# Optimization experiments

Hardware: AMD Instinct MI355X
Metric: run time of the kernel (lower is better)

## Reference

```python
import jax, jax.numpy as jnp
import numpy as np

H = 8
DK = 64          # d_model // h
D_MODEL = 512
DIM_G = 64       # trignometric geometry embedding dim
WAVE_LEN = 1000.0


def box_relational_embedding(boxes):
    # boxes: [B, N, 4] = (x_min, y_min, x_max, y_max)
    x_min, y_min, x_max, y_max = [boxes[..., i:i + 1] for i in range(4)]  # each [B,N,1]
    cx = (x_min + x_max) * 0.5
    cy = (y_min + y_max) * 0.5
    w = (x_max - x_min) + 1.0
    h = (y_max - y_min) + 1.0

    def rel(c, s):
        # log(clamp(|c_i - c_j| / s_i, 1e-3)) -> [B,N,N]
        return jnp.log(jnp.clip(jnp.abs((c - jnp.swapaxes(c, -2, -1)) / s), 1e-3, None))

    delta_x = rel(cx, w)
    delta_y = rel(cy, h)
    delta_w = jnp.log(w / jnp.swapaxes(w, -2, -1))
    delta_h = jnp.log(h / jnp.swapaxes(h, -2, -1))
    pos = jnp.stack([delta_x, delta_y, delta_w, delta_h], axis=-1)  # [B,N,N,4]

    n_freq = DIM_G // 8  # 8 frequencies per geometric feature
    feat_range = jnp.arange(n_freq, dtype=pos.dtype)
    dim_mat = 1.0 / (WAVE_LEN ** (feat_range / n_freq))            # [n_freq]
    mul = (100.0 * pos)[..., None] * dim_mat                        # [B,N,N,4,n_freq]
    B, N = pos.shape[0], pos.shape[1]
    mul = mul.reshape(B, N, N, 4 * n_freq)                          # [B,N,N,32]
    return jnp.concatenate([jnp.sin(mul), jnp.cos(mul)], axis=-1)   # [B,N,N,64]


def setup_inputs() -> dict:
    key = jax.random.key(0)
    ks = jax.random.split(key, 14)
    B, N = 4, 512
    s = 0.02
    return {
        "input_query": jax.random.normal(ks[0], (B, N, D_MODEL), jnp.float32),
        "input_key":   jax.random.normal(ks[1], (B, N, D_MODEL), jnp.float32),
        "input_value": jax.random.normal(ks[2], (B, N, D_MODEL), jnp.float32),
        "input_box":   jax.random.uniform(ks[3], (B, N, 4), jnp.float32),
        "Wq": jax.random.normal(ks[4], (D_MODEL, D_MODEL), jnp.float32) * s,
        "bq": jax.random.normal(ks[5], (D_MODEL,), jnp.float32) * s,
        "Wk": jax.random.normal(ks[6], (D_MODEL, D_MODEL), jnp.float32) * s,
        "bk": jax.random.normal(ks[7], (D_MODEL,), jnp.float32) * s,
        "Wv": jax.random.normal(ks[8], (D_MODEL, D_MODEL), jnp.float32) * s,
        "bv": jax.random.normal(ks[9], (D_MODEL,), jnp.float32) * s,
        "Wo": jax.random.normal(ks[10], (D_MODEL, D_MODEL), jnp.float32) * s,
        "bo": jax.random.normal(ks[11], (D_MODEL,), jnp.float32) * s,
        "WG": jax.random.normal(ks[12], (H, DIM_G), jnp.float32) * s,
        "bG": jax.random.normal(ks[13], (H,), jnp.float32) * s,
    }


def reference(input_query, input_key, input_value, input_box,
              Wq, bq, Wk, bk, Wv, bv, Wo, bo, WG, bG):
    B, N, _ = input_query.shape

    # geometry log-bias per head: relu(Linear_h(emb)) -> [B,H,N,N]
    emb = box_relational_embedding(input_box)                        # [B,N,N,64]
    wg = jax.nn.relu(jnp.einsum('bmng,hg->bhmn', emb, WG)
                     + bG[None, :, None, None])

    def proj(x, W, b):
        # torch Linear: x @ W^T + b, then split heads -> [B,H,N,DK]
        y = x @ W.T + b
        return y.reshape(B, N, H, DK).transpose(0, 2, 1, 3)

    q = proj(input_query, Wq, bq)
    k = proj(input_key, Wk, bk)
    v = proj(input_value, Wv, bv)

    scale = 1.0 / jnp.sqrt(jnp.asarray(DK, q.dtype))
    scores = jnp.einsum('bhqd,bhkd->bhqk', q, k) * scale             # [B,H,N,N]
    logits = jnp.log(jnp.clip(wg, 1e-6, None)) + scores
    attn = jax.nn.softmax(logits, axis=-1)                           # dropout is identity in eval
    out = jnp.einsum('bhqk,bhkd->bhqd', attn, v)
    out = out.transpose(0, 2, 1, 3).reshape(B, N, H * DK)
    return out @ Wo.T + bo
```

## Files before the change

kernel.cpp:

```cpp
#include <hip/hip_runtime.h>
#include <hip/hip_bf16.h>
#include <cstdint>

typedef unsigned short u16;
typedef unsigned int u32;
typedef __attribute__((ext_vector_type(8))) short short8;
typedef __attribute__((ext_vector_type(4))) float f32x4;
typedef __attribute__((ext_vector_type(4))) unsigned int u32x4;
typedef __attribute__((ext_vector_type(4))) unsigned short u16x4;

#define REV 15.91549431f

__device__ __forceinline__ u16 f2b(float x) { return __builtin_bit_cast(u16, (__bf16)x); }
__device__ __forceinline__ u16 f2h(float x) { return __builtin_bit_cast(u16, (_Float16)x); }
__device__ __forceinline__ float c_dim_f(int f) {
    const float c[8] = {1.0f, 0.42169650f, 0.17782794f, 0.074989421f,
                        0.031622777f, 0.013335214f, 0.0056234132f, 0.0023713737f};
    return c[f];
}
__device__ __forceinline__ void gload_lds16(const void* g, void* l) {
    __builtin_amdgcn_global_load_lds((const __attribute__((address_space(1))) u32*)g,
                                     (__attribute__((address_space(3))) u32*)l, 16, 0, 0);
}

__global__ __launch_bounds__(256) void prep_k(const float* __restrict__ s0,
                                              const float* __restrict__ s1,
                                              const float* __restrict__ s2,
                                              const float* __restrict__ s3,
                                              const float* __restrict__ s4,
                                              const float* __restrict__ s5,
                                              const float* __restrict__ s6,
                                              const float* __restrict__ box,
                                              const float* __restrict__ WG,
                                              const float* __restrict__ bG,
                                              u16* __restrict__ dstX,
                                              u16* __restrict__ dstW,
                                              u16* __restrict__ outW) {
    __shared__ char embs[256 * 128];
    const int z = blockIdx.z;
    const int t = threadIdx.x;

    if (z < 7) {
        const float* s;
        u16* dst;
        if (z < 3) {
            s = (z == 0) ? s0 : (z == 1) ? s1 : s2;
            dst = dstX + (size_t)z * 1048576;
        } else {
            if (blockIdx.x >= 256) return;
            s = (z == 3) ? s3 : (z == 4) ? s4 : (z == 5) ? s5 : s6;
            dst = dstW + (size_t)(z - 3) * 262144;
        }
        int i = (blockIdx.x * 256 + t) * 4;
        float4 v = *(const float4*)&s[i];
        u16x4 o = { f2b(v.x), f2b(v.y), f2b(v.z), f2b(v.w) };
        *(u16x4*)&dst[i] = o;
        return;
    }

    if (blockIdx.x >= 256) return;
    const int wave = t >> 6, lane = t & 63;
    const int b = z - 7;
    const int ipair = blockIdx.x;
    const int swz = (t & 7) << 4;

    float cxi[2], cyi[2], wdi[2], hgi[2], lwi[2], lhi[2];
#pragma unroll
    for (int iu = 0; iu < 2; iu++) {
        int ii = (ipair << 1) + iu;
        float4 bi = *(const float4*)&box[(size_t)(((b << 9) + ii) << 2)];
        cxi[iu] = (bi.x + bi.z) * 0.5f; cyi[iu] = (bi.y + bi.w) * 0.5f;
        wdi[iu] = bi.z - bi.x + 1.0f;   hgi[iu] = bi.w - bi.y + 1.0f;
        lwi[iu] = __logf(wdi[iu]);      lhi[iu] = __logf(hgi[iu]);
    }

    const int hh = lane & 15;
    const int ko = (lane >> 4) << 3;
    short8 bf0 = {0,0,0,0,0,0,0,0}, bf1 = {0,0,0,0,0,0,0,0};
    float bGh = 0.0f;
    if (hh < 8) {
        const float* wrow = WG + hh * 64;
#pragma unroll
        for (int e = 0; e < 8; e++) {
            bf0[e] = (short)f2b(wrow[ko + e]);
            bf1[e] = (short)f2b(wrow[32 + ko + e]);
        }
        bGh = bG[hh];
    }

    for (int jt = 0; jt < 2; jt++) {
        const int j = (jt << 8) + t;
        float4 bj = *(const float4*)&box[(size_t)(((b << 9) + j) << 2)];
        float cxj = (bj.x + bj.z) * 0.5f, cyj = (bj.y + bj.w) * 0.5f;
        float wdj = bj.z - bj.x + 1.0f,   hgj = bj.w - bj.y + 1.0f;
        float lwj = __logf(wdj), lhj = __logf(hgj);

#pragma unroll
        for (int iu = 0; iu < 2; iu++) {
            const int ii = (ipair << 1) + iu;
            float pos[4];
            pos[0] = __logf(fmaxf(fabsf((cxi[iu] - cxj) / wdi[iu]), 1e-3f));
            pos[1] = __logf(fmaxf(fabsf((cyi[iu] - cyj) / hgi[iu]), 1e-3f));
            pos[2] = lwi[iu] - lwj;
            pos[3] = lhi[iu] - lhj;

#pragma unroll
            for (int p = 0; p < 4; p++) {
                float rev = pos[p] * REV;
                u32x4 sp, cp;
#pragma unroll
                for (int f = 0; f < 4; f++) {
                    float a0 = rev * c_dim_f(2 * f), a1 = rev * c_dim_f(2 * f + 1);
                    sp[f] = (u32)f2b(__builtin_amdgcn_sinf(a0)) | ((u32)f2b(__builtin_amdgcn_sinf(a1)) << 16);
                    cp[f] = (u32)f2b(__builtin_amdgcn_cosf(a0)) | ((u32)f2b(__builtin_amdgcn_cosf(a1)) << 16);
                }
                *(u32x4*)(embs + (((t << 7) + (p << 4)) ^ swz)) = sp;
                *(u32x4*)(embs + (((t << 7) + 64 + (p << 4)) ^ swz)) = cp;
            }
            __syncthreads();

#pragma unroll
            for (int tt = 0; tt < 4; tt++) {
                int mt = (wave << 2) + tt;
                int row = (mt << 4) + hh;
                int rswz = (row & 7) << 4;
                short8 a0v = *(const short8*)(embs + (((row << 7) + (ko << 1)) ^ rswz));
                short8 a1v = *(const short8*)(embs + (((row << 7) + 64 + (ko << 1)) ^ rswz));
                f32x4 acc = {0.f, 0.f, 0.f, 0.f};
                acc = __builtin_amdgcn_mfma_f32_16x16x32_bf16(a0v, bf0, acc, 0, 0, 0);
                acc = __builtin_amdgcn_mfma_f32_16x16x32_bf16(a1v, bf1, acc, 0, 0, 0);
                if (hh < 8) {
                    int j0 = (jt << 8) + (mt << 4) + ((lane >> 4) << 2);
                    u16x4 ow;
#pragma unroll
                    for (int r = 0; r < 4; r++)
                        ow[r] = f2h(fmaxf(acc[r] + bGh, 1e-6f) * 1024.0f);
                    *(u16x4*)&outW[((size_t)((b << 3) + hh) << 18) + ((size_t)ii << 9) + j0] = ow;
                }
            }
            __syncthreads();
        }
    }
}

__global__ __launch_bounds__(256) void attn_k(const u16* __restrict__ Qb,
                                              const u16* __restrict__ Kb,
                                              const u16* __restrict__ VT,
                                              const u16* __restrict__ Wp,
                                              u16* __restrict__ ATT) {
    __shared__ u16 Pl[4][16 * 68];
    __shared__ float Mrg[3][64][25];
    const int t = threadIdx.x;
    const int wave = t >> 6, lane = t & 63;
    const int c = lane & 15, g = lane >> 4;
    const int bid = blockIdx.x;
    const int qb = bid & 31, bh = bid >> 5;
    const int b = bh >> 3, h = bh & 7;
    const int q0 = qb << 4;

    const u16* Qp = Qb + ((size_t)bh << 15);
    const u16* Kp = Kb + ((size_t)bh << 15);
    const u16* Vp = VT + ((size_t)bh << 15);
    const _Float16* Bp = (const _Float16*)Wp + ((size_t)bh << 18) + ((size_t)q0 << 9);

    short8 qf[2];
#pragma unroll
    for (int ks = 0; ks < 2; ks++)
        qf[ks] = *(const short8*)&Qp[(size_t)(q0 + c) * 64 + ks * 32 + g * 8];

    f32x4 o[4] = {};
    float m[4] = {-1e30f, -1e30f, -1e30f, -1e30f};
    float l[4] = {0.f, 0.f, 0.f, 0.f};

    for (int kt = 0; kt < 2; kt++) {
        const int k0 = ((wave << 1) + kt) << 6;
        short8 kf[4][2], vf[4][2];
#pragma unroll
        for (int jj = 0; jj < 4; jj++)
#pragma unroll
            for (int ks = 0; ks < 2; ks++) {
                kf[jj][ks] = *(const short8*)&Kp[(size_t)(k0 + jj * 16 + c) * 64 + ks * 32 + g * 8];
                vf[jj][ks] = *(const short8*)&Vp[(size_t)(jj * 16 + c) * 512 + k0 + ks * 32 + g * 8];
            }
        float wgt[4][4];
#pragma unroll
        for (int jj = 0; jj < 4; jj++)
#pragma unroll
            for (int r = 0; r < 4; r++)
                wgt[jj][r] = (float)Bp[(size_t)(g * 4 + r) * 512 + k0 + jj * 16 + c];

        f32x4 sa[4] = {};
        __builtin_amdgcn_s_setprio(1);
#pragma unroll
        for (int jj = 0; jj < 4; jj++)
#pragma unroll
            for (int ks = 0; ks < 2; ks++)
                sa[jj] = __builtin_amdgcn_mfma_f32_16x16x32_bf16(qf[ks], kf[jj][ks], sa[jj], 0, 0, 0);
        __builtin_amdgcn_s_setprio(0);

        float s[4][4];
#pragma unroll
        for (int r = 0; r < 4; r++) {
#pragma unroll
            for (int jj = 0; jj < 4; jj++)
                s[jj][r] = sa[jj][r] * 0.125f;
            float v = fmaxf(fmaxf(s[0][r], s[1][r]), fmaxf(s[2][r], s[3][r]));
#pragma unroll
            for (int off = 1; off < 16; off <<= 1)
                v = fmaxf(v, __shfl_xor(v, off));
            float mn = fmaxf(m[r], v);
            float alpha = __expf(m[r] - mn);
            m[r] = mn;
            float rs = 0.f;
#pragma unroll
            for (int jj = 0; jj < 4; jj++) {
                float p = wgt[jj][r] * __expf(s[jj][r] - mn);
                s[jj][r] = p;
                rs += p;
            }
#pragma unroll
            for (int off = 1; off < 16; off <<= 1)
                rs += __shfl_xor(rs, off);
            l[r] = l[r] * alpha + rs;
#pragma unroll
            for (int jjo = 0; jjo < 4; jjo++)
                o[jjo][r] *= alpha;
        }

#pragma unroll
        for (int jj = 0; jj < 4; jj++)
#pragma unroll
            for (int r = 0; r < 4; r++)
                Pl[wave][(g * 4 + r) * 68 + jj * 16 + c] = f2b(s[jj][r]);
        asm volatile("s_waitcnt lgkmcnt(0)" ::: "memory");
        __builtin_amdgcn_sched_barrier(0);

        short8 pa[2];
#pragma unroll
        for (int ks = 0; ks < 2; ks++)
            pa[ks] = *(const short8*)&Pl[wave][c * 68 + ks * 32 + g * 8];
        __builtin_amdgcn_s_setprio(1);
#pragma unroll
        for (int jjo = 0; jjo < 4; jjo++)
#pragma unroll
            for (int ks = 0; ks < 2; ks++)
                o[jjo] = __builtin_amdgcn_mfma_f32_16x16x32_bf16(pa[ks], vf[jjo][ks], o[jjo], 0, 0, 0);
        __builtin_amdgcn_s_setprio(0);
        __builtin_amdgcn_sched_barrier(0);
    }

    if (wave > 0) {
#pragma unroll
        for (int r = 0; r < 4; r++) {
            Mrg[wave - 1][lane][r] = m[r];
            Mrg[wave - 1][lane][4 + r] = l[r];
#pragma unroll
            for (int jjo = 0; jjo < 4; jjo++)
                Mrg[wave - 1][lane][8 + jjo * 4 + r] = o[jjo][r];
        }
    }
    __syncthreads();
    if (wave == 0) {
#pragma unroll
        for (int w = 0; w < 3; w++) {
#pragma unroll
            for (int r = 0; r < 4; r++) {
                float m1 = Mrg[w][lane][r];
                float l1 = Mrg[w][lane][4 + r];
                float mn = fmaxf(m[r], m1);
                float a0 = __expf(m[r] - mn), a1 = __expf(m1 - mn);
                m[r] = mn;
                l[r] = l[r] * a0 + l1 * a1;
#pragma unroll
                for (int jjo = 0; jjo < 4; jjo++)
                    o[jjo][r] = o[jjo][r] * a0 + Mrg[w][lane][8 + jjo * 4 + r] * a1;
            }
        }
#pragma unroll
        for (int r = 0; r < 4; r++) {
            float inv = 1.0f / l[r];
            int row = q0 + g * 4 + r;
#pragma unroll
            for (int jjo = 0; jjo < 4; jjo++)
                ATT[(size_t)(((b << 9) + row) << 9) + (h << 6) + jjo * 16 + c] = f2b(o[jjo][r] * inv);
        }
    }
}

__global__ __launch_bounds__(256) void proj_k(const u16* __restrict__ Xall,
                                              const u16* __restrict__ Wall,
                                              const float* __restrict__ bq,
                                              const float* __restrict__ bk,
                                              const float* __restrict__ bv,
                                              u16* __restrict__ Qb,
                                              u16* __restrict__ Kb,
                                              u16* __restrict__ VT) {
    __shared__ u16 As[2][64 * 32];
    __shared__ u16 Bs[2][64 * 32];

    const int t = threadIdx.x;
    const int wave = t >> 6, lane = t & 63;
    const int wr = wave >> 1, wc = wave & 1;
    const int m0 = blockIdx.y * 64, n0 = blockIdx.x * 64;
    const int z = blockIdx.z;

    const u16* A  = Xall + (size_t)z * 1048576;
    const u16* Bm = Wall + (size_t)z * 262144;
    const float* bias = (z == 0) ? bq : (z == 1) ? bk : bv;
    u16* out = (z == 0) ? Qb : (z == 1) ? Kb : VT;

    f32x4 acc[2][2] = {};
    const int srow = t >> 2;
    const int scol = (((t & 3) ^ ((t >> 3) & 3)) << 3);
    const int c = lane & 15, g = lane >> 4;
    const int gsw = (g ^ ((c >> 1) & 3)) << 3;

    const size_t arow = (size_t)(m0 + srow) * 512 + scol;
    const size_t brow = (size_t)(n0 + srow) * 512 + scol;

    gload_lds16(&A[arow], &As[0][t * 8]);
    gload_lds16(&Bm[brow], &Bs[0][t * 8]);

    int cur = 0;
    for (int k0 = 0; k0 < 512; k0 += 32, cur ^= 1) {
        if (k0 + 32 < 512) {
            gload_lds16(&A[arow + k0 + 32], &As[cur ^ 1][t * 8]);
            gload_lds16(&Bm[brow + k0 + 32], &Bs[cur ^ 1][t * 8]);
            asm volatile("s_waitcnt vmcnt(2)" ::: "memory");
        } else {
            asm volatile("s_waitcnt vmcnt(0)" ::: "memory");
        }
        __builtin_amdgcn_s_barrier();
        __builtin_amdgcn_sched_barrier(0);
        short8 af[2], bfr[2];
#pragma unroll
        for (int i = 0; i < 2; i++)
            af[i] = *(const short8*)&As[cur][(wr * 32 + i * 16 + c) * 32 + gsw];
#pragma unroll
        for (int jj = 0; jj < 2; jj++)
            bfr[jj] = *(const short8*)&Bs[cur][(wc * 32 + jj * 16 + c) * 32 + gsw];
#pragma unroll
        for (int i = 0; i < 2; i++)
#pragma unroll
            for (int jj = 0; jj < 2; jj++)
                acc[i][jj] = __builtin_amdgcn_mfma_f32_16x16x32_bf16(af[i], bfr[jj], acc[i][jj], 0, 0, 0);
        __builtin_amdgcn_sched_barrier(0);
        __builtin_amdgcn_s_barrier();
    }

#pragma unroll
    for (int i = 0; i < 2; i++)
#pragma unroll
        for (int jj = 0; jj < 2; jj++)
#pragma unroll
            for (int r = 0; r < 4; r++) {
                int row = m0 + wr * 32 + i * 16 + ((lane >> 4) << 2) + r;
                int col = n0 + wc * 32 + jj * 16 + (lane & 15);
                float v = acc[i][jj][r] + bias[col];
                int b = row >> 9, rr = row & 511, h = col >> 6, d = col & 63;
                if (z < 2)
                    out[(size_t)((((b << 3) + h) << 9) + rr) * 64 + d] = f2b(v);
                else
                    out[(size_t)((((b << 3) + h) << 6) + d) * 512 + rr] = f2b(v);
            }
}

__global__ __launch_bounds__(256) void outg_k(const u16* __restrict__ A,
                                              const u16* __restrict__ Bm,
                                              const float* __restrict__ bias,
                                              float* __restrict__ outF) {
    __shared__ u16 As[2][64 * 32];
    __shared__ u16 Bs[2][64 * 32];

    const int t = threadIdx.x;
    const int wave = t >> 6, lane = t & 63;
    const int wr = wave >> 1, wc = wave & 1;
    const int m0 = blockIdx.y * 64, n0 = blockIdx.x * 64;

    f32x4 acc[2][2] = {};
    const int srow = t >> 2;
    const int scol = (((t & 3) ^ ((t >> 3) & 3)) << 3);
    const int c = lane & 15, g = lane >> 4;
    const int gsw = (g ^ ((c >> 1) & 3)) << 3;

    const size_t arow = (size_t)(m0 + srow) * 512 + scol;
    const size_t brow = (size_t)(n0 + srow) * 512 + scol;

    gload_lds16(&A[arow], &As[0][t * 8]);
    gload_lds16(&Bm[brow], &Bs[0][t * 8]);

    int cur = 0;
    for (int k0 = 0; k0 < 512; k0 += 32, cur ^= 1) {
        if (k0 + 32 < 512) {
            gload_lds16(&A[arow + k0 + 32], &As[cur ^ 1][t * 8]);
            gload_lds16(&Bm[brow + k0 + 32], &Bs[cur ^ 1][t * 8]);
            asm volatile("s_waitcnt vmcnt(2)" ::: "memory");
        } else {
            asm volatile("s_waitcnt vmcnt(0)" ::: "memory");
        }
        __builtin_amdgcn_s_barrier();
        __builtin_amdgcn_sched_barrier(0);
        short8 af[2], bfr[2];
#pragma unroll
        for (int i = 0; i < 2; i++)
            af[i] = *(const short8*)&As[cur][(wr * 32 + i * 16 + c) * 32 + gsw];
#pragma unroll
        for (int jj = 0; jj < 2; jj++)
            bfr[jj] = *(const short8*)&Bs[cur][(wc * 32 + jj * 16 + c) * 32 + gsw];
#pragma unroll
        for (int i = 0; i < 2; i++)
#pragma unroll
            for (int jj = 0; jj < 2; jj++)
                acc[i][jj] = __builtin_amdgcn_mfma_f32_16x16x32_bf16(af[i], bfr[jj], acc[i][jj], 0, 0, 0);
        __builtin_amdgcn_sched_barrier(0);
        __builtin_amdgcn_s_barrier();
    }

#pragma unroll
    for (int i = 0; i < 2; i++)
#pragma unroll
        for (int jj = 0; jj < 2; jj++)
#pragma unroll
            for (int r = 0; r < 4; r++) {
                int row = m0 + wr * 32 + i * 16 + ((lane >> 4) << 2) + r;
                int col = n0 + wc * 32 + jj * 16 + (lane & 15);
                outF[((size_t)row << 9) + col] = acc[i][jj][r] + bias[col];
            }
}

extern "C" void kernel_launch(void* const* d_in, const int* in_sizes, int n_in,
                              void* d_out, int out_size, void* d_ws, size_t ws_size,
                              hipStream_t stream) {
    const float* inq = (const float*)d_in[0];
    const float* ink = (const float*)d_in[1];
    const float* inv = (const float*)d_in[2];
    const float* box = (const float*)d_in[3];
    const float* Wq  = (const float*)d_in[4];
    const float* bq  = (const float*)d_in[5];
    const float* Wk  = (const float*)d_in[6];
    const float* bk  = (const float*)d_in[7];
    const float* Wv  = (const float*)d_in[8];
    const float* bv  = (const float*)d_in[9];
    const float* Wo  = (const float*)d_in[10];
    const float* bo  = (const float*)d_in[11];
    const float* WG  = (const float*)d_in[12];
    const float* bG  = (const float*)d_in[13];

    u16* base = (u16*)d_ws;
    u16* Xall = base;
    u16* Wall = base + 3145728;
    u16* Qb   = base + 4194304;
    u16* Kb   = base + 5242880;
    u16* VT   = base + 6291456;
    u16* ATT  = base + 7340032;
    u16* Wp   = base + 8388608;

    prep_k<<<dim3(1024, 1, 11), 256, 0, stream>>>(inq, ink, inv, Wq, Wk, Wv, Wo,
                                                  box, WG, bG, Xall, Wall, Wp);

    proj_k<<<dim3(8, 32, 3), 256, 0, stream>>>(Xall, Wall, bq, bk, bv, Qb, Kb, VT);

    attn_k<<<dim3(1024), 256, 0, stream>>>(Qb, Kb, VT, Wp, ATT);

    outg_k<<<dim3(8, 32, 1), 256, 0, stream>>>(ATT, Wall + 786432, bo, (float*)d_out);
}
```

Before: 70.09 us.

## Use single-wave attention blocks that sweep all key tiles without cross-wave merge

The attention kernel now launches one 64-thread wave per query block instead of four waves splitting the key range. Each wave iterates over all eight key tiles with online softmax, which removes the LDS merge of partial max/sum/output and the block barrier. The cost is four times less parallelism per query block and a longer serial loop per wave, so fewer waves are in flight to hide memory latency.

Result: no change. 68.95 us (-1.6%).

```diff
diff --git a/kernel.cpp b/kernel.cpp
--- a/kernel.cpp
+++ b/kernel.cpp
@@ -143,15 +143,13 @@
     }
 }
 
-__global__ __launch_bounds__(256) void attn_k(const u16* __restrict__ Qb,
-                                              const u16* __restrict__ Kb,
-                                              const u16* __restrict__ VT,
-                                              const u16* __restrict__ Wp,
-                                              u16* __restrict__ ATT) {
-    __shared__ u16 Pl[4][16 * 68];
-    __shared__ float Mrg[3][64][25];
-    const int t = threadIdx.x;
-    const int wave = t >> 6, lane = t & 63;
+__global__ __launch_bounds__(64) void attn_k(const u16* __restrict__ Qb,
+                                             const u16* __restrict__ Kb,
+                                             const u16* __restrict__ VT,
+                                             const u16* __restrict__ Wp,
+                                             u16* __restrict__ ATT) {
+    __shared__ u16 Pl[16 * 68];
+    const int lane = threadIdx.x;
     const int c = lane & 15, g = lane >> 4;
     const int bid = blockIdx.x;
     const int qb = bid & 31, bh = bid >> 5;
@@ -172,8 +170,8 @@
     float m[4] = {-1e30f, -1e30f, -1e30f, -1e30f};
     float l[4] = {0.f, 0.f, 0.f, 0.f};
 
-    for (int kt = 0; kt < 2; kt++) {
-        const int k0 = ((wave << 1) + kt) << 6;
+    for (int kt = 0; kt < 8; kt++) {
+        const int k0 = kt << 6;
         short8 kf[4][2], vf[4][2];
 #pragma unroll
         for (int jj = 0; jj < 4; jj++)
@@ -231,14 +229,14 @@
         for (int jj = 0; jj < 4; jj++)
 #pragma unroll
             for (int r = 0; r < 4; r++)
-                Pl[wave][(g * 4 + r) * 68 + jj * 16 + c] = f2b(s[jj][r]);
+                Pl[(g * 4 + r) * 68 + jj * 16 + c] = f2b(s[jj][r]);
         asm volatile("s_waitcnt lgkmcnt(0)" ::: "memory");
         __builtin_amdgcn_sched_barrier(0);
 
         short8 pa[2];
 #pragma unroll
         for (int ks = 0; ks < 2; ks++)
-            pa[ks] = *(const short8*)&Pl[wave][c * 68 + ks * 32 + g * 8];
+            pa[ks] = *(const short8*)&Pl[c * 68 + ks * 32 + g * 8];
         __builtin_amdgcn_s_setprio(1);
 #pragma unroll
         for (int jjo = 0; jjo < 4; jjo++)
@@ -249,41 +247,13 @@
         __builtin_amdgcn_sched_barrier(0);
     }
 
-    if (wave > 0) {
-#pragma unroll
-        for (int r = 0; r < 4; r++) {
-            Mrg[wave - 1][lane][r] = m[r];
-            Mrg[wave - 1][lane][4 + r] = l[r];
-#pragma unroll
-            for (int jjo = 0; jjo < 4; jjo++)
-                Mrg[wave - 1][lane][8 + jjo * 4 + r] = o[jjo][r];
-        }
-    }
-    __syncthreads();
-    if (wave == 0) {
-#pragma unroll
-        for (int w = 0; w < 3; w++) {
-#pragma unroll
-            for (int r = 0; r < 4; r++) {
-                float m1 = Mrg[w][lane][r];
-                float l1 = Mrg[w][lane][4 + r];
-                float mn = fmaxf(m[r], m1);
-                float a0 = __expf(m[r] - mn), a1 = __expf(m1 - mn);
-                m[r] = mn;
-                l[r] = l[r] * a0 + l1 * a1;
-#pragma unroll
-                for (int jjo = 0; jjo < 4; jjo++)
-                    o[jjo][r] = o[jjo][r] * a0 + Mrg[w][lane][8 + jjo * 4 + r] * a1;
-            }
-        }
-#pragma unroll
-        for (int r = 0; r < 4; r++) {
-            float inv = 1.0f / l[r];
-            int row = q0 + g * 4 + r;
-#pragma unroll
-            for (int jjo = 0; jjo < 4; jjo++)
-                ATT[(size_t)(((b << 9) + row) << 9) + (h << 6) + jjo * 16 + c] = f2b(o[jjo][r] * inv);
-        }
+#pragma unroll
+    for (int r = 0; r < 4; r++) {
+        float inv = 1.0f / l[r];
+        int row = q0 + g * 4 + r;
+#pragma unroll
+        for (int jjo = 0; jjo < 4; jjo++)
+            ATT[(size_t)(((b << 9) + row) << 9) + (h << 6) + jjo * 16 + c] = f2b(o[jjo][r] * inv);
     }
 }
 
@@ -460,7 +430,7 @@
 
     proj_k<<<dim3(8, 32, 3), 256, 0, stream>>>(Xall, Wall, bq, bk, bv, Qb, Kb, VT);
 
-    attn_k<<<dim3(1024), 256, 0, stream>>>(Qb, Kb, VT, Wp, ATT);
+    attn_k<<<dim3(1024), 64, 0, stream>>>(Qb, Kb, VT, Wp, ATT);
 
     outg_k<<<dim3(8, 32, 1), 256, 0, stream>>>(ATT, Wall + 786432, bo, (float*)d_out);
 }
```
